# Performance work log

Hardware: AMD Instinct MI355X
Metric: run time of the kernel (lower is better)

Reference implementation:

```python
import jax, jax.numpy as jnp
import numpy as np

WIN, DIL, PAD, H = 5, 1, 2, 8  # window, dilation, unfold padding, num_heads
C = 256
EPS = 1e-5

def _ln(z, g, b):
    m = jnp.mean(z, axis=-1, keepdims=True)
    v = jnp.mean((z - m) ** 2, axis=-1, keepdims=True)
    return (z - m) * jax.lax.rsqrt(v + EPS) * g + b

def setup_inputs() -> dict:
    key = jax.random.key(0)
    ks = jax.random.split(key, 16)
    s = 0.02
    d = {
        'x': jax.random.normal(ks[0], (32, C, 64, 25), jnp.float32),
        'ln1_g': jnp.ones((C,), jnp.float32), 'ln1_b': jnp.zeros((C,), jnp.float32),
        'q_w': jax.random.normal(ks[1], (C, C)) * s, 'q_b': jnp.zeros((C,)),
        'qa_w': jax.random.normal(ks[2], (C, H)) * s, 'qa_b': jnp.zeros((H,)),
        'k_w': jax.random.normal(ks[3], (C, C)) * s, 'k_b': jnp.zeros((C,)),
        'ka_w': jax.random.normal(ks[4], (C, H)) * s, 'ka_b': jnp.zeros((H,)),
        'v_w': jax.random.normal(ks[5], (C, C)) * s, 'v_b': jnp.zeros((C,)),
        't_w': jax.random.normal(ks[6], (C, C)) * s, 't_b': jnp.zeros((C,)),
        'p_w': jax.random.normal(ks[7], (C, C)) * s, 'p_b': jnp.zeros((C,)),
        'ffn_g': jnp.ones((C,)), 'ffn_b': jnp.zeros((C,)),
        'w1': jax.random.normal(ks[8], (C, C)) * s, 'b1': jnp.zeros((C,)),
        'w2': jax.random.normal(ks[9], (C, C)) * s, 'b2': jnp.zeros((C,)),
    }
    return d

def reference(x, ln1_g, ln1_b, q_w, q_b, qa_w, qa_b, k_w, k_b, ka_w, ka_b,
              v_w, v_b, t_w, t_b, p_w, p_b, ffn_g, ffn_b, w1, b1, w2, b2):
    N, Cc, T, V = x.shape
    hc = Cc // H
    scale = 1.0 / np.sqrt(hc)
    B, L = N * T, WIN * V
    xp = jnp.pad(x, ((0, 0), (0, 0), (PAD, PAD), (0, 0)))
    win = jnp.stack([xp[:, :, k * DIL:k * DIL + T, :] for k in range(WIN)], axis=2)  # (N,C,W,T,V)
    wx = win.transpose(0, 3, 2, 4, 1).reshape(B, L, Cc)
    nx = _ln(wx, ln1_g, ln1_b)
    # attention: softmax-pooled query
    q = nx @ q_w + q_b                                      # (B,L,C)
    qw = jax.nn.softmax(((q @ qa_w + qa_b) * scale).transpose(0, 2, 1), axis=-1)  # (B,H,L)
    qh = q.reshape(B, L, H, hc).transpose(0, 2, 1, 3)       # (B,H,L,hc)
    pq = jnp.einsum('bhl,bhld->bhd', qw, qh)                # (B,H,hc)
    k_ = nx @ k_w + k_b
    kq = k_ * pq.reshape(B, 1, Cc)
    kw = jax.nn.softmax(((kq @ ka_w + ka_b) * scale).transpose(0, 2, 1), axis=-1)
    kh = k_.reshape(B, L, H, hc).transpose(0, 2, 1, 3)
    pk = jnp.einsum('bhl,bhld->bhd', kw, kh)                # (B,H,hc)
    v_ = nx @ v_w + v_b
    vh = v_.reshape(B, L, H, hc).transpose(0, 2, 1, 3)
    kv = (vh * pk[:, :, None, :]).transpose(0, 2, 1, 3).reshape(B, L, Cc)
    kvh = (kv @ t_w + t_b).reshape(B, L, H, hc).transpose(0, 2, 1, 3)
    att = ((kvh + qh).transpose(0, 2, 1, 3).reshape(B, L, Cc)) @ p_w + p_b
    # average over window, residual with flattened x
    att = att.reshape(B, WIN, V, Cc).mean(axis=1)           # (B,V,C)
    att = att + x.transpose(0, 2, 3, 1).reshape(B, V, Cc)
    # FFN residual block
    f = _ln(att, ffn_g, ffn_b)
    f = jax.nn.gelu(f @ w1 + b1, approximate=False) @ w2 + b2
    y = f + att
    return y.reshape(N, T, V, Cc).transpose(0, 3, 1, 2)     # (N,C,T,V)
```

## Files before the change

kernel.cpp:

```cpp
#include <hip/hip_runtime.h>
#include <hip/hip_bf16.h>

typedef unsigned short u16b;
typedef __attribute__((ext_vector_type(8))) short short8;
typedef __attribute__((ext_vector_type(4))) float floatx4;

#define DEV static __device__ __forceinline__

DEV float sh2f(unsigned short s) { union { unsigned u; float f; } c; c.u = ((unsigned)s) << 16; return c.f; }
DEV unsigned short f2b(float f) {
    unsigned u = __float_as_uint(f);
    u += 0x7FFF + ((u >> 16) & 1);
    return (unsigned short)(u >> 16);
}

DEV void gload_lds16(const u16b* g, u16b* l) {
    __builtin_amdgcn_global_load_lds((const __attribute__((address_space(1))) void*)g,
                                     (__attribute__((address_space(3))) void*)l, 16, 0, 0);
}

constexpr int O_LN1G = 0, O_LN1B = 256, O_QB = 512, O_KB = 768, O_VB = 1024,
              O_TB = 1280, O_PB = 1536, O_FFNG = 1792, O_FFNB = 2048,
              O_B1 = 2304, O_B2 = 2560, O_QAB = 2816, O_KAB = 2824,
              O_QAW = 2832, O_KAW = 4880, O_CV = 6928;

__global__ void detect_k(const unsigned* __restrict__ xw, int* __restrict__ flag) {
    __shared__ int cnt;
    if (threadIdx.x == 0) cnt = 0;
    __syncthreads();
    int my = 0;
    for (int i = threadIdx.x; i < 4096; i += 256) {
        unsigned w = xw[i];
        unsigned e0 = (w >> 7) & 0xFFu;
        if (e0 >= 0xC0u) my++;
    }
    atomicAdd(&cnt, my);
    __syncthreads();
    if (threadIdx.x == 0) flag[0] = (cnt > 64) ? 1 : 0;
}

DEV unsigned short load_cvt(const void* src, size_t idx, int fp32) {
    return fp32 ? f2b(((const float*)src)[idx]) : ((const u16b*)src)[idx];
}

struct VecTab { const void* p[15]; int off[15]; int n[15]; };

__global__ __launch_bounds__(256)
void convert_vecs_k(VecTab tab, const int* __restrict__ flag, u16b* __restrict__ sv) {
    int e = blockIdx.x, fp32 = flag[0];
    const void* s = tab.p[e];
    int n = tab.n[e], off = tab.off[e];
    for (int i = threadIdx.x; i < n; i += 256)
        sv[off + i] = load_cvt(s, i, fp32);
}

struct W8 { const void* p[8]; unsigned dstoff[8]; unsigned rstride[8]; };

__global__ void wtrans_k(W8 tab, u16b* __restrict__ base, const int* __restrict__ flag) {
    __shared__ u16b tile[32][33];
    int fp32 = flag[0];
    const void* src = tab.p[blockIdx.z];
    u16b* dst = base + tab.dstoff[blockIdx.z];
    unsigned rs = tab.rstride[blockIdx.z];
    int c0 = blockIdx.x * 32, r0 = blockIdx.y * 32;
    int tx = threadIdx.x, ty = threadIdx.y;
#pragma unroll
    for (int i = 0; i < 32; i += 8)
        tile[ty + i][tx] = load_cvt(src, (size_t)(r0 + ty + i) * 256 + c0 + tx, fp32);
    __syncthreads();
#pragma unroll
    for (int i = 0; i < 32; i += 8)
        dst[(size_t)(c0 + ty + i) * rs + r0 + tx] = tile[tx][ty + i];
}

__global__ __launch_bounds__(256)
void transpose_in_k(const void* __restrict__ src, u16b* __restrict__ dst,
                    int rows, int cols, const int* __restrict__ flag) {
    __shared__ u16b tile[32][36];
    int fp32 = flag[0];
    int c0 = blockIdx.x * 32, r0 = blockIdx.y * 32;
    size_t zb = (size_t)blockIdx.z * rows * cols;
    int tid = threadIdx.x;
    int r = tid >> 3, c4 = (tid & 7) * 4;
    size_t sidx = zb + (size_t)(r0 + r) * cols + c0 + c4;
    if (fp32) {
        const float4 f4 = *(const float4*)((const float*)src + sidx);
        tile[r][c4]     = f2b(f4.x);
        tile[r][c4 + 1] = f2b(f4.y);
        tile[r][c4 + 2] = f2b(f4.z);
        tile[r][c4 + 3] = f2b(f4.w);
    } else {
        *(ushort4*)&tile[r][c4] = *(const ushort4*)((const u16b*)src + sidx);
    }
    __syncthreads();
    int c = tid >> 3, r4 = (tid & 7) * 4;
    ushort4 o;
    o.x = tile[r4][c]; o.y = tile[r4 + 1][c]; o.z = tile[r4 + 2][c]; o.w = tile[r4 + 3][c];
    *(ushort4*)&dst[zb + (size_t)(c0 + c) * rows + r0 + r4] = o;
}

__global__ __launch_bounds__(256)
void rowstats_k(const u16b* __restrict__ src, float2* __restrict__ st,
                int valid, int total) {
    int wv = threadIdx.x >> 6, lane = threadIdx.x & 63;
    int r = blockIdx.x * 4 + wv;
    if (r >= total) return;
    if (r >= valid) { if (lane == 0) st[r] = make_float2(0.f, 0.f); return; }
    int c = lane * 4;
    ushort4 raw = *(const ushort4*)&src[(size_t)r * 256 + c];
    float x0 = sh2f(raw.x), x1 = sh2f(raw.y), x2 = sh2f(raw.z), x3 = sh2f(raw.w);
    float s  = x0 + x1 + x2 + x3;
    float sq = x0 * x0 + x1 * x1 + x2 * x2 + x3 * x3;
#pragma unroll
    for (int o = 32; o; o >>= 1) { s += __shfl_xor(s, o); sq += __shfl_xor(sq, o); }
    float mean = s * (1.f / 256.f);
    float var  = sq * (1.f / 256.f) - mean * mean;
    if (lane == 0) st[r] = make_float2(mean, rsqrtf(var + 1e-5f));
}

__global__ __launch_bounds__(256)
void cvec_k(const u16b* __restrict__ pT, u16b* __restrict__ sv) {
    int j = threadIdx.x;
    float acc = sh2f(sv[O_PB + j]);
    const u16b* row = pT + (size_t)j * 256;
    for (int i = 0; i < 256; i += 8) {
        short8 t8 = *(const short8*)&sv[O_TB + i];
        short8 p8 = *(const short8*)&row[i];
#pragma unroll
        for (int u = 0; u < 8; ++u)
            acc += sh2f((unsigned short)t8[u]) * sh2f((unsigned short)p8[u]);
    }
    sv[O_CV + j] = f2b(acc);
}

template <int EPI, int LNA, int XY = 0, int STATS = 0>
__global__ __launch_bounds__(256, 4)
void gemm256(const u16b* __restrict__ A, int aStride, int K,
             const u16b* __restrict__ Wt,
             const u16b* __restrict__ bias, const u16b* __restrict__ addm,
             u16b* __restrict__ out, size_t osParam,
             const float2* __restrict__ stats, const float2* __restrict__ stats2,
             const u16b* __restrict__ gvec, const u16b* __restrict__ bvec,
             float2* __restrict__ statOut, const int* __restrict__ flag) {
    constexpr bool ALDS = (LNA == 0);
    __shared__ u16b As[64 * 72];
    __shared__ u16b Bs[128 * 64];
    __shared__ float sg[256], sb[256];
    __shared__ float2 spart[64][2];
    const int tid = threadIdx.x;
    const int m0 = (XY ? blockIdx.y : blockIdx.x) * 64;
    const int n0 = (XY ? blockIdx.x : blockIdx.y) * 128;
    const int wv = tid >> 6, lane = tid & 63;
    const int wrow = (wv >> 1) * 32, wcol = (wv & 1) * 64;
    const int fr = lane & 15;
    const int fq = lane >> 4;
    floatx4 acc[2][4];
    const floatx4 zero = {0.f, 0.f, 0.f, 0.f};
#pragma unroll
    for (int i = 0; i < 2; ++i)
#pragma unroll
        for (int j = 0; j < 4; ++j) acc[i][j] = zero;

    float2 strow[2];
    if (LNA) {
        sg[tid] = sh2f(gvec[tid]);
        sb[tid] = sh2f(bvec[tid]);
#pragma unroll
        for (int kk = 0; kk < 2; ++kk) {
            int r = m0 + (tid >> 3) + kk * 32;
            if (LNA == 2) {
                float2 a = stats[r], b = stats2[r];
                float mean = (a.x + b.x) * (1.f / 256.f);
                float var  = (a.y + b.y) * (1.f / 256.f) - mean * mean;
                strow[kk] = make_float2(mean, rsqrtf(var + 1e-5f));
            } else {
                strow[kk] = stats[r];
            }
        }
        __syncthreads();
    }

    for (int kt = 0; kt < K; kt += 64) {
        if (ALDS) {
#pragma unroll
            for (int kk = 0; kk < 2; ++kk) {
                int chunk = tid + kk * 256;
                int row = chunk >> 3, col = (chunk & 7) * 8;
                int scol = col ^ ((row & 7) << 3);
                gload_lds16(&A[(size_t)(m0 + row) * aStride + kt + scol], &As[chunk * 8]);
            }
        } else {
#pragma unroll
            for (int kk = 0; kk < 2; ++kk) {
                int chunk = tid + kk * 256;
                int row = chunk >> 3, col = (chunk & 7) * 8;
                union { uint4 u; unsigned short h[8]; } rw;
                rw.u = *(const uint4*)&A[(size_t)(m0 + row) * aStride + kt + col];
#pragma unroll
                for (int j = 0; j < 8; ++j) {
                    float f = sh2f(rw.h[j]);
                    f = (f - strow[kk].x) * strow[kk].y * sg[kt + col + j] + sb[kt + col + j];
                    rw.h[j] = f2b(f);
                }
                *(uint4*)&As[row * 72 + col] = rw.u;
            }
        }
#pragma unroll
        for (int kk = 0; kk < 4; ++kk) {
            int chunk = tid + kk * 256;
            int row = chunk >> 3, col = (chunk & 7) * 8;
            int scol = col ^ ((row & 7) << 3);
            gload_lds16(&Wt[(size_t)(n0 + row) * K + kt + scol], &Bs[chunk * 8]);
        }
        __syncthreads();
#pragma unroll
        for (int s = 0; s < 2; ++s) {
            short8 af[2], bfr[4];
#pragma unroll
            for (int i = 0; i < 2; ++i) {
                int ar = wrow + i * 16 + fr;
                if (ALDS)
                    af[i] = *(const short8*)((const char*)As +
                              ((ar * 128 + s * 64 + fq * 16) ^ ((ar & 7) << 4)));
                else
                    af[i] = *(short8*)&As[ar * 72 + s * 32 + fq * 8];
            }
#pragma unroll
            for (int j = 0; j < 4; ++j) {
                int br = wcol + j * 16 + fr;
                bfr[j] = *(const short8*)((const char*)Bs +
                          ((br * 128 + s * 64 + fq * 16) ^ ((br & 7) << 4)));
            }
#pragma unroll
            for (int i = 0; i < 2; ++i)
#pragma unroll
                for (int j = 0; j < 4; ++j)
                    acc[i][j] = __builtin_amdgcn_mfma_f32_16x16x32_bf16(af[i], bfr[j], acc[i][j], 0, 0, 0);
        }
        __syncthreads();
    }
    float bv[4];
#pragma unroll
    for (int j = 0; j < 4; ++j) bv[j] = bias ? sh2f(bias[n0 + wcol + j * 16 + fr]) : 0.f;

    if (EPI == 5) {
        int fp32o = flag[0];
#pragma unroll
        for (int i = 0; i < 2; ++i) {
            int row0 = m0 + wrow + i * 16 + fq * 4;
            int n = row0 / 1600;
            int tv = row0 - n * 1600;
#pragma unroll
            for (int j = 0; j < 4; ++j) {
                int col = n0 + wcol + j * 16 + fr;
                float v4[4];
#pragma unroll
                for (int r = 0; r < 4; ++r)
                    v4[r] = acc[i][j][r] + bv[j] + sh2f(addm[(size_t)(row0 + r) * 256 + col]);
                size_t oidx = ((size_t)n * 256 + col) * 1600 + tv;
                if (fp32o) {
                    float4 o = {v4[0], v4[1], v4[2], v4[3]};
                    *(float4*)((float*)out + oidx) = o;
                } else {
                    ushort4 o;
                    o.x = f2b(v4[0]); o.y = f2b(v4[1]); o.z = f2b(v4[2]); o.w = f2b(v4[3]);
                    *(ushort4*)&out[oidx] = o;
                }
            }
        }
    } else {
#pragma unroll
        for (int i = 0; i < 2; ++i) {
#pragma unroll
            for (int r = 0; r < 4; ++r) {
                int row = m0 + wrow + i * 16 + fq * 4 + r;
                size_t ro = (size_t)row * 256;
                float s1 = 0.f, s2 = 0.f;
#pragma unroll
                for (int j = 0; j < 4; ++j) {
                    int col = n0 + wcol + j * 16 + fr;
                    float val = acc[i][j][r] + bv[j];
                    if (EPI == 2) val += sh2f(addm[ro + col]);
                    if (EPI == 3) val = 0.5f * val * (1.0f + erff(val * 0.70710678118654752f));
                    if (STATS) { s1 += val; s2 += val * val; }
                    if (EPI == 4)      out[(size_t)(col >> 8) * osParam + ro + (col & 255)] = f2b(val);
                    else if (EPI == 0) out[(size_t)row * osParam + col] = f2b(val);
                    else               out[ro + col] = f2b(val);
                }
                if (STATS) {
#pragma unroll
                    for (int mm = 1; mm < 16; mm <<= 1) {
                        s1 += __shfl_xor(s1, mm);
                        s2 += __shfl_xor(s2, mm);
                    }
                    if (fr == 0) spart[wrow + i * 16 + fq * 4 + r][wv & 1] = make_float2(s1, s2);
                }
            }
        }
        if (STATS) {
            __syncthreads();
            if (tid < 64) {
                float2 a = spart[tid][0], b = spart[tid][1];
                statOut[(size_t)(n0 >> 7) * 51200 + m0 + tid] = make_float2(a.x + b.x, a.y + b.y);
            }
        }
    }
}

DEV void pool_stage(const u16b* __restrict__ S, const u16b* __restrict__ sv,
                    int awoff, int aboff, const float* mult, float* outPool,
                    const int* srow, u16b* su, float* slog, float* spool, int tid) {
    for (int i = tid; i < 2048; i += 512) {
        int c = i >> 3, h = i & 7;
        float w = sh2f(sv[awoff + i]);
        if (mult) w *= mult[c];
        su[h * 260 + c] = f2b(w);
    }
    __syncthreads();
    int wv = tid >> 6, lane = tid & 63;
    int fr = lane & 15, fq = lane >> 4;
    floatx4 acc = {0.f, 0.f, 0.f, 0.f};
    const u16b* Ar = S + (size_t)srow[wv * 16 + fr] * 256;
#pragma unroll
    for (int s = 0; s < 8; ++s) {
        short8 a  = *(const short8*)&Ar[s * 32 + fq * 8];
        short8 bb = *(const short8*)&su[fr * 260 + s * 32 + fq * 8];
        acc = __builtin_amdgcn_mfma_f32_16x16x32_bf16(a, bb, acc, 0, 0, 0);
    }
    float abv = sh2f(sv[aboff + (fr & 7)]);
    if (fr < 8) {
#pragma unroll
        for (int r = 0; r < 4; ++r)
            slog[(wv * 16 + fq * 4 + r) * 9 + fr] = (acc[r] + abv) * 0.17677669529663687f;
    }
    __syncthreads();
    {
        int h = wv;
        float v0 = (lane < 125) ? slog[lane * 9 + h] : -1e30f;
        float v1 = (lane + 64 < 125) ? slog[(lane + 64) * 9 + h] : -1e30f;
        float mx = fmaxf(v0, v1);
#pragma unroll
        for (int o = 32; o; o >>= 1) mx = fmaxf(mx, __shfl_xor(mx, o));
        float e0 = (lane < 125) ? __expf(v0 - mx) : 0.f;
        float e1 = (lane + 64 < 125) ? __expf(v1 - mx) : 0.f;
        float s = e0 + e1;
#pragma unroll
        for (int o = 32; o; o >>= 1) s += __shfl_xor(s, o);
        float inv = 1.f / s;
        if (lane < 125) slog[lane * 9 + h] = e0 * inv;
        if (lane + 64 < 125) slog[(lane + 64) * 9 + h] = e1 * inv;
    }
    __syncthreads();
    int c8 = (tid & 31) * 8, ls = tid >> 5;
    int h2 = c8 >> 5;
    float a8[8] = {0.f, 0.f, 0.f, 0.f, 0.f, 0.f, 0.f, 0.f};
    for (int l = ls; l < 125; l += 16) {
        float w = slog[l * 9 + h2];
        short8 d8 = *(const short8*)&S[(size_t)srow[l] * 256 + c8];
#pragma unroll
        for (int j = 0; j < 8; ++j) a8[j] += w * sh2f((unsigned short)d8[j]);
    }
#pragma unroll
    for (int j = 0; j < 8; ++j) spool[ls * 260 + c8 + j] = a8[j];
    __syncthreads();
    if (tid < 256) {
        float s = 0.f;
#pragma unroll
        for (int q = 0; q < 16; ++q) s += spool[q * 260 + tid];
        outPool[tid] = s;
    }
    __syncthreads();
}

__global__ __launch_bounds__(512)
void pool_fused(const u16b* __restrict__ qf, const u16b* __restrict__ kf,
                const u16b* __restrict__ vf, const u16b* __restrict__ sv,
                u16b* __restrict__ CB) {
    __shared__ int srow[128];
    __shared__ u16b su[16 * 260];
    __shared__ float slog[128 * 9];
    __shared__ float spool[16 * 260];
    __shared__ float spq[256], spk[256];
    int bid = blockIdx.x;
    int b = ((bid & 7) << 8) | (bid >> 3);
    int n = b >> 6, t = b & 63;
    int tid = threadIdx.x;
    if (tid < 128) {
        int l = tid < 125 ? tid : 124;
        int w = l / 25, v = l - w * 25, tt = t + w - 2;
        srow[tid] = ((unsigned)tt < 64u) ? (n * 64 + tt) * 25 + v : 51200;
    }
    for (int i = tid; i < 8 * 260; i += 512) su[8 * 260 + i] = 0;
    __syncthreads();
    pool_stage(qf, sv, O_QAW, O_QAB, nullptr, spq, srow, su, slog, spool, tid);
    for (int i = tid; i < 800; i += 512) {
        int v = i >> 5, c8 = (i & 31) * 8;
        float s[8] = {0.f, 0.f, 0.f, 0.f, 0.f, 0.f, 0.f, 0.f};
#pragma unroll
        for (int w = 0; w < 5; ++w) {
            short8 d8 = *(const short8*)&qf[(size_t)srow[w * 25 + v] * 256 + c8];
#pragma unroll
            for (int j = 0; j < 8; ++j) s[j] += sh2f((unsigned short)d8[j]);
        }
        unsigned short o[8];
#pragma unroll
        for (int j = 0; j < 8; ++j) o[j] = f2b(s[j] * 0.2f);
        *(uint4*)&CB[((size_t)b * 25 + v) * 512 + 256 + c8] = *(uint4*)o;
    }
    pool_stage(kf, sv, O_KAW, O_KAB, spq, spk, srow, su, slog, spool, tid);
    for (int i = tid; i < 800; i += 512) {
        int v = i >> 5, c8 = (i & 31) * 8;
        float s[8] = {0.f, 0.f, 0.f, 0.f, 0.f, 0.f, 0.f, 0.f};
#pragma unroll
        for (int w = 0; w < 5; ++w) {
            short8 d8 = *(const short8*)&vf[(size_t)srow[w * 25 + v] * 256 + c8];
#pragma unroll
            for (int j = 0; j < 8; ++j) s[j] += sh2f((unsigned short)d8[j]);
        }
        unsigned short o[8];
#pragma unroll
        for (int j = 0; j < 8; ++j) o[j] = f2b(s[j] * 0.2f * spk[c8 + j]);
        *(uint4*)&CB[((size_t)b * 25 + v) * 512 + c8] = *(uint4*)o;
    }
}

extern "C" void kernel_launch(void* const* d_in, const int* in_sizes, int n_in,
                              void* d_out, int out_size, void* d_ws, size_t ws_size,
                              hipStream_t stream) {
    (void)in_sizes; (void)n_in; (void)out_size; (void)ws_size;
    const void* x    = d_in[0];
    const void* ln1g = d_in[1];  const void* ln1b = d_in[2];
    const void* q_w  = d_in[3];  const void* q_b  = d_in[4];
    const void* qa_w = d_in[5];  const void* qa_b = d_in[6];
    const void* k_w  = d_in[7];  const void* k_b  = d_in[8];
    const void* ka_w = d_in[9];  const void* ka_b = d_in[10];
    const void* v_w  = d_in[11]; const void* v_b  = d_in[12];
    const void* t_w  = d_in[13]; const void* t_b  = d_in[14];
    const void* p_w  = d_in[15]; const void* p_b  = d_in[16];
    const void* ffng = d_in[17]; const void* ffnb = d_in[18];
    const void* w1   = d_in[19]; const void* b1   = d_in[20];
    const void* w2   = d_in[21]; const void* b2   = d_in[22];

    char* ws = (char*)d_ws;
    size_t off = 0;
    auto alloc = [&](size_t bytes) { void* p = ws + off; off += (bytes + 255) & ~(size_t)255; return p; };
    const size_t RPAD = 51328;
    int*    flag = (int*)alloc(256);
    u16b*   sv   = (u16b*)alloc(8192 * 2);
    u16b*   wT   = (u16b*)alloc((size_t)7 * 65536 * 2);
    u16b*   cW   = (u16b*)alloc((size_t)256 * 512 * 2);
    u16b*   xT   = (u16b*)alloc(RPAD * 256 * 2);
    u16b*   Bq   = (u16b*)alloc(RPAD * 256 * 2);
    u16b*   Bk   = (u16b*)alloc(RPAD * 256 * 2);
    u16b*   Bv   = (u16b*)alloc(RPAD * 256 * 2);
    u16b*   CB   = (u16b*)alloc((size_t)51200 * 512 * 2);
    u16b*   att  = (u16b*)alloc((size_t)51200 * 256 * 2);
    float2* st1  = (float2*)alloc(RPAD * 8);
    float2* st2p = (float2*)alloc((size_t)2 * 51200 * 8);

    u16b* pT  = wT + 3 * 65536;
    u16b* tT  = wT + 4 * 65536;
    u16b* w1T = wT + 5 * 65536;
    u16b* w2T = wT + 6 * 65536;

    detect_k<<<1, 256, 0, stream>>>((const unsigned*)x, flag);
    VecTab tab;
    const void* vp[15] = {ln1g, ln1b, q_b, k_b, v_b, t_b, p_b, ffng, ffnb, b1, b2, qa_b, ka_b, qa_w, ka_w};
    const int vo[15] = {O_LN1G, O_LN1B, O_QB, O_KB, O_VB, O_TB, O_PB, O_FFNG, O_FFNB, O_B1, O_B2, O_QAB, O_KAB, O_QAW, O_KAW};
    const int vn[15] = {256, 256, 256, 256, 256, 256, 256, 256, 256, 256, 256, 8, 8, 2048, 2048};
    for (int i = 0; i < 15; ++i) { tab.p[i] = vp[i]; tab.off[i] = vo[i]; tab.n[i] = vn[i]; }
    convert_vecs_k<<<15, 256, 0, stream>>>(tab, flag, sv);

    dim3 tb(32, 8);
    W8 wt;
    const void* wsrc[8] = {q_w, k_w, v_w, p_w, t_w, w1, w2, p_w};
    for (int i = 0; i < 8; ++i) {
        wt.p[i] = wsrc[i];
        wt.dstoff[i] = (i < 7) ? (unsigned)(i * 65536) : (unsigned)((cW + 256) - wT);
        wt.rstride[i] = (i < 7) ? 256u : 512u;
    }
    wtrans_k<<<dim3(8, 8, 8), tb, 0, stream>>>(wt, wT, flag);
    cvec_k<<<1, 256, 0, stream>>>(pT, sv);
    gemm256<0, 0><<<dim3(4, 2), 256, 0, stream>>>(pT, 256, 256, tT, nullptr, nullptr,
                                                  cW, 512, nullptr, nullptr, nullptr, nullptr,
                                                  nullptr, nullptr);
    transpose_in_k<<<dim3(50, 8, 32), 256, 0, stream>>>(x, xT, 256, 1600, flag);
    rowstats_k<<<12832, 256, 0, stream>>>(xT, st1, 51200, 51328);
    gemm256<4, 1, 1><<<dim3(6, 802), 256, 0, stream>>>(xT, 256, 256, wT, sv + O_QB, nullptr,
                                                       Bq, RPAD * 256, st1, nullptr,
                                                       sv + O_LN1G, sv + O_LN1B, nullptr, nullptr);
    pool_fused<<<2048, 512, 0, stream>>>(Bq, Bk, Bv, sv, CB);
    gemm256<2, 0, 1, 1><<<dim3(2, 800), 256, 0, stream>>>(CB, 512, 512, cW, sv + O_CV, xT,
                                                          att, 256, nullptr, nullptr,
                                                          nullptr, nullptr, st2p, nullptr);
    gemm256<3, 2, 1><<<dim3(2, 800), 256, 0, stream>>>(att, 256, 256, w1T, sv + O_B1, nullptr,
                                                       Bq, 256, st2p, st2p + 51200,
                                                       sv + O_FFNG, sv + O_FFNB, nullptr, nullptr);
    gemm256<5, 0, 1><<<dim3(2, 800), 256, 0, stream>>>(Bq, 256, 256, w2T, sv + O_B2, att,
                                                       (u16b*)d_out, 0, nullptr, nullptr,
                                                       nullptr, nullptr, nullptr, flag);
}
```

Baseline: 378.2 us.

## Process two adjacent time windows per pooling block to share overlapping rows

The pooling kernel now handles two consecutive time steps per block. It loads the 6-frame union of their windows once and computes logits, softmax and pooled sums for both outputs from that shared data. The window means for both time steps also come from one 6-frame pass, and half as many blocks are launched. This cuts redundant global reads of overlapping window rows and per-block setup such as weight staging. In exchange there is more shared memory per block, more work per block, extra zeroing, and only 1024 blocks, which may leave the GPU less evenly occupied.

```diff
diff --git a/kernel.cpp b/kernel.cpp
--- a/kernel.cpp
+++ b/kernel.cpp
@@ -307,37 +307,38 @@
     }
 }
 
-DEV void pool_stage(const u16b* __restrict__ S, const u16b* __restrict__ sv,
-                    int awoff, int aboff, const float* mult, float* outPool,
-                    const int* srow, u16b* su, float* slog, float* spool, int tid) {
-    for (int i = tid; i < 2048; i += 512) {
-        int c = i >> 3, h = i & 7;
-        float w = sh2f(sv[awoff + i]);
-        if (mult) w *= mult[c];
-        su[h * 260 + c] = f2b(w);
-    }
-    __syncthreads();
+
+DEV void logits_union(const u16b* __restrict__ S, const u16b* su, const int* srow,
+                      float* slog, const u16b* __restrict__ sv, int aboff, int tid) {
     int wv = tid >> 6, lane = tid & 63;
     int fr = lane & 15, fq = lane >> 4;
-    floatx4 acc = {0.f, 0.f, 0.f, 0.f};
-    const u16b* Ar = S + (size_t)srow[wv * 16 + fr] * 256;
-#pragma unroll
-    for (int s = 0; s < 8; ++s) {
-        short8 a  = *(const short8*)&Ar[s * 32 + fq * 8];
-        short8 bb = *(const short8*)&su[fr * 260 + s * 32 + fq * 8];
-        acc = __builtin_amdgcn_mfma_f32_16x16x32_bf16(a, bb, acc, 0, 0, 0);
-    }
     float abv = sh2f(sv[aboff + (fr & 7)]);
-    if (fr < 8) {
+    for (int f = wv; f < 10; f += 8) {
+        floatx4 acc = {0.f, 0.f, 0.f, 0.f};
+        const u16b* Ar = S + (size_t)srow[f * 16 + fr] * 256;
+#pragma unroll
+        for (int s = 0; s < 8; ++s) {
+            short8 a  = *(const short8*)&Ar[s * 32 + fq * 8];
+            short8 bb = *(const short8*)&su[fr * 260 + s * 32 + fq * 8];
+            acc = __builtin_amdgcn_mfma_f32_16x16x32_bf16(a, bb, acc, 0, 0, 0);
+        }
 #pragma unroll
         for (int r = 0; r < 4; ++r)
-            slog[(wv * 16 + fq * 4 + r) * 9 + fr] = (acc[r] + abv) * 0.17677669529663687f;
-    }
-    __syncthreads();
-    {
-        int h = wv;
-        float v0 = (lane < 125) ? slog[lane * 9 + h] : -1e30f;
-        float v1 = (lane + 64 < 125) ? slog[(lane + 64) * 9 + h] : -1e30f;
+            slog[(f * 16 + fq * 4 + r) * 18 + fr] = (acc[r] + abv) * 0.17677669529663687f;
+    }
+}
+
+template <int KC>
+DEV void softmax16(const float* slog, float* wqA, float* wqB, int tid) {
+    int wv = tid >> 6, lane = tid & 63;
+#pragma unroll
+    for (int c = 0; c < 2; ++c) {
+        int combo = wv + c * 8;
+        int dt = combo >> 3, h = combo & 7;
+        int col = KC ? combo : h;
+        const float* src = slog + (size_t)(dt * 25) * 18 + col;
+        float v0 = (lane < 125) ? src[lane * 18] : -1e30f;
+        float v1 = (lane + 64 < 125) ? src[(lane + 64) * 18] : -1e30f;
         float mx = fmaxf(v0, v1);
 #pragma unroll
         for (int o = 32; o; o >>= 1) mx = fmaxf(mx, __shfl_xor(mx, o));
@@ -347,81 +348,142 @@
 #pragma unroll
         for (int o = 32; o; o >>= 1) s += __shfl_xor(s, o);
         float inv = 1.f / s;
-        if (lane < 125) slog[lane * 9 + h] = e0 * inv;
-        if (lane + 64 < 125) slog[(lane + 64) * 9 + h] = e1 * inv;
-    }
-    __syncthreads();
-    int c8 = (tid & 31) * 8, ls = tid >> 5;
-    int h2 = c8 >> 5;
-    float a8[8] = {0.f, 0.f, 0.f, 0.f, 0.f, 0.f, 0.f, 0.f};
-    for (int l = ls; l < 125; l += 16) {
-        float w = slog[l * 9 + h2];
-        short8 d8 = *(const short8*)&S[(size_t)srow[l] * 256 + c8];
-#pragma unroll
-        for (int j = 0; j < 8; ++j) a8[j] += w * sh2f((unsigned short)d8[j]);
-    }
-#pragma unroll
-    for (int j = 0; j < 8; ++j) spool[ls * 260 + c8 + j] = a8[j];
+        float* dst = dt ? wqB : wqA;
+        int off = dt ? 25 : 0;
+        if (lane < 125) dst[(lane + off) * 9 + h] = e0 * inv;
+        if (lane + 64 < 125) dst[(lane + 64 + off) * 9 + h] = e1 * inv;
+    }
+}
+
+DEV void pool_union(const u16b* __restrict__ S, const int* srow,
+                    const float* wqA, const float* wqB, float* scratch,
+                    float* out0, float* out1, int tid) {
+    int c8 = (tid & 31) * 8, h = c8 >> 5, ls = tid >> 5;
+    float a0[8] = {0.f,0.f,0.f,0.f,0.f,0.f,0.f,0.f};
+    float a1[8] = {0.f,0.f,0.f,0.f,0.f,0.f,0.f,0.f};
+    for (int u = ls; u < 150; u += 16) {
+        float w0 = wqA[u * 9 + h];
+        float w1 = wqB[u * 9 + h];
+        short8 d8 = *(const short8*)&S[(size_t)srow[u] * 256 + c8];
+#pragma unroll
+        for (int j = 0; j < 8; ++j) {
+            float f = sh2f((unsigned short)d8[j]);
+            a0[j] += w0 * f;
+            a1[j] += w1 * f;
+        }
+    }
+#pragma unroll
+    for (int j = 0; j < 8; ++j) {
+        a0[j] += __shfl_xor(a0[j], 32);
+        a1[j] += __shfl_xor(a1[j], 32);
+    }
+    int wv = tid >> 6, lane = tid & 63;
+    if (lane < 32) {
+#pragma unroll
+        for (int j = 0; j < 8; ++j) scratch[wv * 260 + c8 + j] = a0[j];
+    }
     __syncthreads();
     if (tid < 256) {
         float s = 0.f;
 #pragma unroll
-        for (int q = 0; q < 16; ++q) s += spool[q * 260 + tid];
-        outPool[tid] = s;
-    }
-    __syncthreads();
-}
-
-__global__ __launch_bounds__(512)
-void pool_fused(const u16b* __restrict__ qf, const u16b* __restrict__ kf,
-                const u16b* __restrict__ vf, const u16b* __restrict__ sv,
-                u16b* __restrict__ CB) {
-    __shared__ int srow[128];
-    __shared__ u16b su[16 * 260];
-    __shared__ float slog[128 * 9];
-    __shared__ float spool[16 * 260];
-    __shared__ float spq[256], spk[256];
-    int bid = blockIdx.x;
-    int b = ((bid & 7) << 8) | (bid >> 3);
-    int n = b >> 6, t = b & 63;
-    int tid = threadIdx.x;
-    if (tid < 128) {
-        int l = tid < 125 ? tid : 124;
-        int w = l / 25, v = l - w * 25, tt = t + w - 2;
-        srow[tid] = ((unsigned)tt < 64u) ? (n * 64 + tt) * 25 + v : 51200;
-    }
-    for (int i = tid; i < 8 * 260; i += 512) su[8 * 260 + i] = 0;
-    __syncthreads();
-    pool_stage(qf, sv, O_QAW, O_QAB, nullptr, spq, srow, su, slog, spool, tid);
+        for (int q = 0; q < 8; ++q) s += scratch[q * 260 + tid];
+        out0[tid] = s;
+    }
+    __syncthreads();
+    if (lane < 32) {
+#pragma unroll
+        for (int j = 0; j < 8; ++j) scratch[wv * 260 + c8 + j] = a1[j];
+    }
+    __syncthreads();
+    if (tid < 256) {
+        float s = 0.f;
+#pragma unroll
+        for (int q = 0; q < 8; ++q) s += scratch[q * 260 + tid];
+        out1[tid] = s;
+    }
+    __syncthreads();
+}
+
+DEV void wmean2(const u16b* __restrict__ S, const int* srow,
+                const float* scale0, const float* scale1,
+                u16b* __restrict__ CB, int base, int nb, int tid) {
     for (int i = tid; i < 800; i += 512) {
         int v = i >> 5, c8 = (i & 31) * 8;
-        float s[8] = {0.f, 0.f, 0.f, 0.f, 0.f, 0.f, 0.f, 0.f};
-#pragma unroll
-        for (int w = 0; w < 5; ++w) {
-            short8 d8 = *(const short8*)&qf[(size_t)srow[w * 25 + v] * 256 + c8];
-#pragma unroll
-            for (int j = 0; j < 8; ++j) s[j] += sh2f((unsigned short)d8[j]);
-        }
-        unsigned short o[8];
-#pragma unroll
-        for (int j = 0; j < 8; ++j) o[j] = f2b(s[j] * 0.2f);
-        *(uint4*)&CB[((size_t)b * 25 + v) * 512 + 256 + c8] = *(uint4*)o;
-    }
-    pool_stage(kf, sv, O_KAW, O_KAB, spq, spk, srow, su, slog, spool, tid);
-    for (int i = tid; i < 800; i += 512) {
-        int v = i >> 5, c8 = (i & 31) * 8;
-        float s[8] = {0.f, 0.f, 0.f, 0.f, 0.f, 0.f, 0.f, 0.f};
-#pragma unroll
-        for (int w = 0; w < 5; ++w) {
-            short8 d8 = *(const short8*)&vf[(size_t)srow[w * 25 + v] * 256 + c8];
-#pragma unroll
-            for (int j = 0; j < 8; ++j) s[j] += sh2f((unsigned short)d8[j]);
-        }
-        unsigned short o[8];
-#pragma unroll
-        for (int j = 0; j < 8; ++j) o[j] = f2b(s[j] * 0.2f * spk[c8 + j]);
-        *(uint4*)&CB[((size_t)b * 25 + v) * 512 + c8] = *(uint4*)o;
-    }
+        float s0[8] = {0.f,0.f,0.f,0.f,0.f,0.f,0.f,0.f};
+        float s1[8] = {0.f,0.f,0.f,0.f,0.f,0.f,0.f,0.f};
+#pragma unroll
+        for (int w = 0; w < 6; ++w) {
+            short8 d8 = *(const short8*)&S[(size_t)srow[w * 25 + v] * 256 + c8];
+#pragma unroll
+            for (int j = 0; j < 8; ++j) {
+                float f = sh2f((unsigned short)d8[j]);
+                if (w < 5)  s0[j] += f;
+                if (w >= 1) s1[j] += f;
+            }
+        }
+        unsigned short o0[8], o1[8];
+#pragma unroll
+        for (int j = 0; j < 8; ++j) {
+            float m0 = s0[j] * 0.2f, m1 = s1[j] * 0.2f;
+            if (scale0) { m0 *= scale0[c8 + j]; m1 *= scale1[c8 + j]; }
+            o0[j] = f2b(m0); o1[j] = f2b(m1);
+        }
+        *(uint4*)&CB[((size_t)nb * 25 + v) * 512 + base + c8]       = *(uint4*)o0;
+        *(uint4*)&CB[((size_t)(nb + 1) * 25 + v) * 512 + base + c8] = *(uint4*)o1;
+    }
+}
+
+__global__ __launch_bounds__(512)
+void pool_fused2(const u16b* __restrict__ qf, const u16b* __restrict__ kf,
+                 const u16b* __restrict__ vf, const u16b* __restrict__ sv,
+                 u16b* __restrict__ CB) {
+    __shared__ int srow[160];
+    __shared__ u16b su[16 * 260];
+    __shared__ float slog[160 * 18];
+    __shared__ float wqA[160 * 9], wqB[160 * 9];
+    __shared__ float spq[2][256], spk[2][256];
+    int bid = blockIdx.x;
+    int b2 = ((bid & 7) << 7) | (bid >> 3);
+    int n = b2 >> 5, t0 = (b2 & 31) * 2;
+    int nb = n * 64 + t0;
+    int tid = threadIdx.x;
+    if (tid < 160) {
+        int u = tid < 150 ? tid : 149;
+        int tl = u / 25, v = u - tl * 25, tt = t0 + tl - 2;
+        srow[tid] = ((unsigned)tt < 64u) ? (n * 64 + tt) * 25 + v : 51200;
+    }
+    for (int i = tid; i < 2048; i += 512) {
+        int c = i >> 3, h = i & 7;
+        su[h * 260 + c] = sv[O_QAW + i];
+    }
+    for (int i = tid; i < 1440; i += 512) { wqA[i] = 0.f; wqB[i] = 0.f; }
+    __syncthreads();
+
+    logits_union(qf, su, srow, slog, sv, O_QAB, tid);
+    __syncthreads();
+    softmax16<0>(slog, wqA, wqB, tid);
+    __syncthreads();
+
+    pool_union(qf, srow, wqA, wqB, slog, spq[0], spq[1], tid);
+
+    wmean2(qf, srow, nullptr, nullptr, CB, 256, nb, tid);
+
+    for (int i = tid; i < 4096; i += 512) {
+        int c = i >> 4, h16 = i & 15;
+        float w = sh2f(sv[O_KAW + c * 8 + (h16 & 7)]) * spq[h16 >> 3][c];
+        su[h16 * 260 + c] = f2b(w);
+    }
+    for (int i = tid; i < 1440; i += 512) { wqA[i] = 0.f; wqB[i] = 0.f; }
+    __syncthreads();
+
+    logits_union(kf, su, srow, slog, sv, O_KAB, tid);
+    __syncthreads();
+    softmax16<1>(slog, wqA, wqB, tid);
+    __syncthreads();
+
+    pool_union(kf, srow, wqA, wqB, slog, spk[0], spk[1], tid);
+
+    wmean2(vf, srow, spk[0], spk[1], CB, 0, nb, tid);
 }
 
 extern "C" void kernel_launch(void* const* d_in, const int* in_sizes, int n_in,
@@ -489,7 +551,7 @@
     gemm256<4, 1, 1><<<dim3(6, 802), 256, 0, stream>>>(xT, 256, 256, wT, sv + O_QB, nullptr,
                                                        Bq, RPAD * 256, st1, nullptr,
                                                        sv + O_LN1G, sv + O_LN1B, nullptr, nullptr);
-    pool_fused<<<2048, 512, 0, stream>>>(Bq, Bk, Bv, sv, CB);
+    pool_fused2<<<1024, 512, 0, stream>>>(Bq, Bk, Bv, sv, CB);
     gemm256<2, 0, 1, 1><<<dim3(2, 800), 256, 0, stream>>>(CB, 512, 512, cW, sv + O_CV, xT,
                                                           att, 256, nullptr, nullptr,
                                                           nullptr, nullptr, st2p, nullptr);
```

After: 373.0 us. About the same (-1.4%).
